# Kernel optimization log

Measured on AMD Instinct MI355X. Metric: run time of the kernel, lower is better.

## Reference

```python
import jax, jax.numpy as jnp
import numpy as np

B, C, D = 32768, 1000, 512
ALPHA, BETA = 1.0, 1.0
TEMPERATURE = 0.1


def setup_inputs() -> dict:
    key = jax.random.key(0)
    k1, k2, k3, k4 = jax.random.split(key, 4)
    return {
        "features_front": jax.random.normal(k1, (B, D), dtype=jnp.float32),
        "logits": jax.random.normal(k2, (B, C), dtype=jnp.float32),
        "labels": jax.random.randint(k3, (B,), 0, C, dtype=jnp.int64),
        "text_prototype": jax.random.normal(k4, (C, D), dtype=jnp.float32),
    }


def reference(features_front, logits, labels, text_prototype):
    num_class = text_prototype.shape[0]

    # F.cross_entropy (mean reduction)
    logp = jax.nn.log_softmax(logits, axis=-1)
    loss_ce = -jnp.mean(jnp.take_along_axis(logp, labels[:, None], axis=1)[:, 0])

    # F.normalize(prototypes, dim=1)
    norm = jnp.linalg.norm(text_prototype, axis=1, keepdims=True)
    prototypes = text_prototype / jnp.maximum(norm, 1e-12)

    # supervised contrastive term against class prototypes
    feat_dot_prototype = (features_front @ prototypes.T) / TEMPERATURE  # [B, C]
    logits_max = jax.lax.stop_gradient(jnp.max(feat_dot_prototype, axis=1, keepdims=True))
    lg = feat_dot_prototype - logits_max
    log_prob = lg - jnp.log(jnp.sum(jnp.exp(lg), axis=1, keepdims=True))
    mask = (labels[:, None] == jnp.arange(num_class)[None, :]).astype(log_prob.dtype)
    mean_log_prob_pos = jnp.sum(mask * log_prob, axis=1)
    simloss = -jnp.mean(mean_log_prob_pos)

    # prototype repulsion: sum_{i != j} exp(p_i . p_j) == masked exp-sum of Gram matrix
    gram = prototypes @ prototypes.T  # [C, C]
    offdiag = 1.0 - jnp.eye(num_class, dtype=gram.dtype)
    textloss = jnp.log(jnp.sum(jnp.exp(gram) * offdiag)) / num_class

    return ALPHA * simloss + BETA * loss_ce + textloss
```

## Files before the change

kernel.cpp:

```cpp
#include <hip/hip_runtime.h>
#include <math.h>

#define NB 32768
#define NC 1000
#define ND 512
#define NTILES 63
#define LOG2E 1.4426950408889634f
#define LN2 0.6931471805599453f
#define S2 14.426950408889634f
#define NBUCKET 64

typedef __attribute__((ext_vector_type(8))) short short8;
typedef __attribute__((ext_vector_type(4))) float f32x4;

__device__ __forceinline__ float fexp2(float x) {
    float r; asm("v_exp_f32 %0, %1" : "=v"(r) : "v"(x)); return r;
}
__device__ __forceinline__ float flog2(float x) {
    float r; asm("v_log_f32 %0, %1" : "=v"(r) : "v"(x)); return r;
}
__device__ __forceinline__ unsigned short bf16_rne(float f) {
    unsigned int u = __builtin_bit_cast(unsigned int, f);
    u += 0x7FFFu + ((u >> 16) & 1u);
    return (unsigned short)(u >> 16);
}
__device__ __forceinline__ short8 pack8f(float4 a, float4 b) {
    short8 s;
    s[0] = (short)bf16_rne(a.x); s[1] = (short)bf16_rne(a.y);
    s[2] = (short)bf16_rne(a.z); s[3] = (short)bf16_rne(a.w);
    s[4] = (short)bf16_rne(b.x); s[5] = (short)bf16_rne(b.y);
    s[6] = (short)bf16_rne(b.z); s[7] = (short)bf16_rne(b.w);
    return s;
}

__global__ __launch_bounds__(256) void norm_protos(const float* __restrict__ pro,
                                                   unsigned short* __restrict__ pbf) {
    const int row = blockIdx.x, t = threadIdx.x;
    const int tile = row >> 4, r = row & 15;
    const int kk = t >> 4, g = (t >> 2) & 3, slot = t & 3;
    unsigned int* dst = (unsigned int*)pbf +
        ((size_t)tile * 1024 + kk * 64 + g * 16 + r) * 4 + slot;
    if (row >= NC) { *dst = 0u; return; }
    const float* rp = pro + (size_t)row * ND;
    const float x0 = rp[2 * t], x1 = rp[2 * t + 1];
    float ss = x0 * x0 + x1 * x1;
#pragma unroll
    for (int o = 1; o < 64; o <<= 1) ss += __shfl_xor(ss, o, 64);
    __shared__ float part[4];
    if ((t & 63) == 0) part[t >> 6] = ss;
    __syncthreads();
    const float nrm = sqrtf(part[0] + part[1] + part[2] + part[3]);
    const float sc = 1.0f / fmaxf(nrm, 1e-12f);
    *dst = (unsigned int)bf16_rne(x0 * sc) | ((unsigned int)bf16_rne(x1 * sc) << 16);
}

#define TILE_BODY(P, CT)                                                            \
    do {                                                                            \
        f32x4 a0 = {0.f, 0.f, 0.f, 0.f}, a1 = {0.f, 0.f, 0.f, 0.f};                \
        _Pragma("unroll")                                                           \
        for (int kk = 0; kk < 16; ++kk) {                                           \
            a0 = __builtin_amdgcn_mfma_f32_16x16x32_bf16(P[kk], bf0[kk], a0, 0, 0, 0); \
            a1 = __builtin_amdgcn_mfma_f32_16x16x32_bf16(P[kk], bf1[kk], a1, 0, 0, 0); \
        }                                                                           \
        const int cbase = (CT) * 16 + g * 4;                                        \
        {                                                                           \
            float x[4];                                                            \
            _Pragma("unroll")                                                       \
            for (int rI = 0; rI < 4; ++rI) {                                        \
                const float v = a0[rI] * S2;                                        \
                x[rI] = (cbase + rI < NC) ? v : -INFINITY;                          \
                lv0 += (cbase + rI == lab0) ? v : 0.f;                              \
            }                                                                       \
            const float tmax = fmaxf(fmaxf(x[0], x[1]), fmaxf(x[2], x[3]));         \
            const float mn = fmaxf(m0, tmax);                                       \
            ls0 *= fexp2(m0 - mn);                                                  \
            m0 = mn;                                                                \
            ls0 += fexp2(x[0] - mn) + fexp2(x[1] - mn) + fexp2(x[2] - mn) + fexp2(x[3] - mn); \
        }                                                                           \
        {                                                                           \
            float x[4];                                                            \
            _Pragma("unroll")                                                       \
            for (int rI = 0; rI < 4; ++rI) {                                        \
                const float v = a1[rI] * S2;                                        \
                x[rI] = (cbase + rI < NC) ? v : -INFINITY;                          \
                lv1 += (cbase + rI == lab1) ? v : 0.f;                              \
            }                                                                       \
            const float tmax = fmaxf(fmaxf(x[0], x[1]), fmaxf(x[2], x[3]));         \
            const float mn = fmaxf(m1, tmax);                                       \
            ls1 *= fexp2(m1 - mn);                                                  \
            m1 = mn;                                                                \
            ls1 += fexp2(x[0] - mn) + fexp2(x[1] - mn) + fexp2(x[2] - mn) + fexp2(x[3] - mn); \
        }                                                                           \
    } while (0)

__global__ __launch_bounds__(256, 1) void main_kernel(const float* __restrict__ feat,
                                                      const float* __restrict__ logits,
                                                      const int* __restrict__ labels,
                                                      const unsigned short* __restrict__ pbf,
                                                      float* __restrict__ buckets) {
    __shared__ float wsum[4], wsumce[4];
    const int t = threadIdx.x;
    const int wid = t >> 6, lane = t & 63;
    const int r16 = lane & 15, g = lane >> 4;
    const int rowbase = blockIdx.x * 128 + wid * 32;
    const short8* frag = (const short8*)pbf;

    short8 PA[16], PB[16];
#pragma unroll
    for (int k = 0; k < 16; ++k) PA[k] = frag[k * 64 + lane];

    short8 bf0[16], bf1[16];
    {
        const float* f0 = feat + (size_t)(rowbase + r16) * ND + 8 * g;
        const float* f1 = f0 + 16 * ND;
#pragma unroll
        for (int kk = 0; kk < 16; ++kk) {
            bf0[kk] = pack8f(*(const float4*)(f0 + 32 * kk), *(const float4*)(f0 + 32 * kk + 4));
            bf1[kk] = pack8f(*(const float4*)(f1 + 32 * kk), *(const float4*)(f1 + 32 * kk + 4));
        }
    }
    int lab0 = labels[rowbase + r16];
    int lab1 = labels[rowbase + 16 + r16];
    lab0 = lab0 < 0 ? 0 : (lab0 > NC - 1 ? NC - 1 : lab0);
    lab1 = lab1 < 0 ? 0 : (lab1 > NC - 1 ? NC - 1 : lab1);

    float m0 = -INFINITY, ls0 = 0.f, lv0 = 0.f;
    float m1 = -INFINITY, ls1 = 0.f, lv1 = 0.f;

#pragma unroll 1
    for (int ct = 0; ct < 62; ct += 2) {
#pragma unroll
        for (int k = 0; k < 16; ++k) PB[k] = frag[(ct + 1) * 1024 + k * 64 + lane];
        TILE_BODY(PA, ct);
#pragma unroll
        for (int k = 0; k < 16; ++k) PA[k] = frag[(ct + 2) * 1024 + k * 64 + lane];
        TILE_BODY(PB, ct + 1);
    }
    TILE_BODY(PA, 62);

#pragma unroll
    for (int o = 16; o <= 32; o <<= 1) {
        {
            const float mo = __shfl_xor(m0, o, 64), lo = __shfl_xor(ls0, o, 64);
            lv0 += __shfl_xor(lv0, o, 64);
            const float mm = fmaxf(m0, mo);
            ls0 = ls0 * fexp2(m0 - mm) + lo * fexp2(mo - mm);
            m0 = mm;
        }
        {
            const float mo = __shfl_xor(m1, o, 64), lo = __shfl_xor(ls1, o, 64);
            lv1 += __shfl_xor(lv1, o, 64);
            const float mm = fmaxf(m1, mo);
            ls1 = ls1 * fexp2(m1 - mm) + lo * fexp2(mo - mm);
            m1 = mm;
        }
    }
    const float row0 = (m0 + flog2(ls0) - lv0) * LN2;
    const float row1 = (m1 + flog2(ls1) - lv1) * LN2;
    float mine = (row0 + row1) * (1.0f / (4.0f * (float)NB));
#pragma unroll
    for (int o = 1; o < 64; o <<= 1) mine += __shfl_xor(mine, o, 64);

    float localce = 0.f;
#pragma unroll 1
    for (int i = 0; i < 32; ++i) {
        const int row = rowbase + i;
        const float* rp = logits + (size_t)row * NC;
        float x[16];
#pragma unroll
        for (int j = 0; j < 4; ++j) {
            const int c0 = lane * 4 + j * 256;
            if (c0 < NC) {
                const float4 v = *(const float4*)(rp + c0);
                x[4 * j] = v.x * LOG2E; x[4 * j + 1] = v.y * LOG2E;
                x[4 * j + 2] = v.z * LOG2E; x[4 * j + 3] = v.w * LOG2E;
            } else {
                x[4 * j] = x[4 * j + 1] = x[4 * j + 2] = x[4 * j + 3] = -INFINITY;
            }
        }
        float m = -INFINITY;
#pragma unroll
        for (int i2 = 0; i2 < 16; ++i2) m = fmaxf(m, x[i2]);
#pragma unroll
        for (int o = 1; o < 64; o <<= 1) m = fmaxf(m, __shfl_xor(m, o, 64));
        float s = 0.f;
#pragma unroll
        for (int i2 = 0; i2 < 16; ++i2) s += fexp2(x[i2] - m);
#pragma unroll
        for (int o = 1; o < 64; o <<= 1) s += __shfl_xor(s, o, 64);
        int lab = labels[row];
        lab = lab < 0 ? 0 : (lab > NC - 1 ? NC - 1 : lab);
        localce += (m + flog2(s)) * LN2 - rp[lab];
    }

    if (lane == 0) { wsum[wid] = mine; wsumce[wid] = localce; }
    __syncthreads();
    if (t == 0) {
        const int b = (blockIdx.x & (NBUCKET - 1)) * 16;
        atomicAdd(buckets + b, wsum[0] + wsum[1] + wsum[2] + wsum[3]);
        atomicAdd(buckets + 1024 + b,
                  (wsumce[0] + wsumce[1] + wsumce[2] + wsumce[3]) * (1.0f / (float)NB));
    }
}

__global__ __launch_bounds__(256) void gram_kernel(const unsigned short* __restrict__ pbf,
                                                   float* __restrict__ buckets) {
    __shared__ float wsum[4];
    const int t = threadIdx.x;
    const int wid = t >> 6, lane = t & 63;
    const int r16 = lane & 15, g = lane >> 4;
    const int ct = blockIdx.y;
    const int btile = blockIdx.x * 4 + wid;
    const int irow = btile * 16 + r16;
    const short8* frag = (const short8*)pbf;

    short8 af[16], bf[16];
#pragma unroll
    for (int kk = 0; kk < 16; ++kk) {
        af[kk] = frag[(size_t)ct * 1024 + kk * 64 + lane];
        bf[kk] = frag[(size_t)btile * 1024 + kk * 64 + lane];
    }
    f32x4 dacc = {0.f, 0.f, 0.f, 0.f};
#pragma unroll
    for (int kk = 0; kk < 16; ++kk)
        dacc = __builtin_amdgcn_mfma_f32_16x16x32_bf16(af[kk], bf[kk], dacc, 0, 0, 0);

    float s = 0.f;
    if (irow < NC) {
        const int cbase = ct * 16 + g * 4;
#pragma unroll
        for (int rI = 0; rI < 4; ++rI) {
            const int j = cbase + rI;
            if (j < NC && j != irow) s += fexp2(dacc[rI] * LOG2E);
        }
    }
#pragma unroll
    for (int o = 1; o < 64; o <<= 1) s += __shfl_xor(s, o, 64);
    if (lane == 0) wsum[wid] = s;
    __syncthreads();
    if (t == 0)
        atomicAdd(buckets + ((blockIdx.x + 16 * blockIdx.y) & (NBUCKET - 1)) * 16,
                  wsum[0] + wsum[1] + wsum[2] + wsum[3]);
}

__global__ void combine_kernel(const float* __restrict__ a, float* __restrict__ out) {
    const int t = threadIdx.x;
    float s = a[t * 16], c = a[1024 + t * 16], gr = a[2048 + t * 16];
#pragma unroll
    for (int o = 1; o < 64; o <<= 1) {
        s += __shfl_xor(s, o, 64);
        c += __shfl_xor(c, o, 64);
        gr += __shfl_xor(gr, o, 64);
    }
    if (t == 0) out[0] = s + c + logf(gr) * (1.0f / (float)NC);
}

extern "C" void kernel_launch(void* const* d_in, const int* in_sizes, int n_in,
                              void* d_out, int out_size, void* d_ws, size_t ws_size,
                              hipStream_t stream) {
    const float* feat   = (const float*)d_in[0];
    const float* logits = (const float*)d_in[1];
    const int*   labels = (const int*)d_in[2];
    const float* pro    = (const float*)d_in[3];
    float* out = (float*)d_out;

    float* acc = (float*)d_ws;
    unsigned short* pbf = (unsigned short*)((char*)d_ws + 16384);

    hipMemsetAsync(d_ws, 0, 3072 * sizeof(float), stream);
    hipLaunchKernelGGL(norm_protos,    dim3(1024),     dim3(256), 0, stream, pro, pbf);
    hipLaunchKernelGGL(main_kernel,    dim3(NB / 128), dim3(256), 0, stream, feat, logits, labels, pbf, acc);
    hipLaunchKernelGGL(gram_kernel,    dim3(16, 63),   dim3(256), 0, stream, pbf, acc + 2048);
    hipLaunchKernelGGL(combine_kernel, dim3(1),        dim3(64),  0, stream, acc, out);
}
```

Before: 101.2 us.

## Halve rows per wave and split K-half prefetch to raise main kernel occupancy

Each wave now handles 16 feature rows instead of 32, and the grid doubles to NB/64 blocks. The prototype tile is prefetched in two K-halves of 8 fragments, with two partial MFMA accumulators summed afterwards. This cuts register use so launch bounds can ask for 2 blocks per CU, meant to hide memory latency better. The cross-entropy loop handles two rows per iteration for more ILP. The trade-off is that each prototype tile is reloaded by twice as many waves, and each MFMA chain is shorter.

```diff
diff --git a/kernel.cpp b/kernel.cpp
--- a/kernel.cpp
+++ b/kernel.cpp
@@ -54,46 +54,7 @@
     *dst = (unsigned int)bf16_rne(x0 * sc) | ((unsigned int)bf16_rne(x1 * sc) << 16);
 }
 
-#define TILE_BODY(P, CT)                                                            \
-    do {                                                                            \
-        f32x4 a0 = {0.f, 0.f, 0.f, 0.f}, a1 = {0.f, 0.f, 0.f, 0.f};                \
-        _Pragma("unroll")                                                           \
-        for (int kk = 0; kk < 16; ++kk) {                                           \
-            a0 = __builtin_amdgcn_mfma_f32_16x16x32_bf16(P[kk], bf0[kk], a0, 0, 0, 0); \
-            a1 = __builtin_amdgcn_mfma_f32_16x16x32_bf16(P[kk], bf1[kk], a1, 0, 0, 0); \
-        }                                                                           \
-        const int cbase = (CT) * 16 + g * 4;                                        \
-        {                                                                           \
-            float x[4];                                                            \
-            _Pragma("unroll")                                                       \
-            for (int rI = 0; rI < 4; ++rI) {                                        \
-                const float v = a0[rI] * S2;                                        \
-                x[rI] = (cbase + rI < NC) ? v : -INFINITY;                          \
-                lv0 += (cbase + rI == lab0) ? v : 0.f;                              \
-            }                                                                       \
-            const float tmax = fmaxf(fmaxf(x[0], x[1]), fmaxf(x[2], x[3]));         \
-            const float mn = fmaxf(m0, tmax);                                       \
-            ls0 *= fexp2(m0 - mn);                                                  \
-            m0 = mn;                                                                \
-            ls0 += fexp2(x[0] - mn) + fexp2(x[1] - mn) + fexp2(x[2] - mn) + fexp2(x[3] - mn); \
-        }                                                                           \
-        {                                                                           \
-            float x[4];                                                            \
-            _Pragma("unroll")                                                       \
-            for (int rI = 0; rI < 4; ++rI) {                                        \
-                const float v = a1[rI] * S2;                                        \
-                x[rI] = (cbase + rI < NC) ? v : -INFINITY;                          \
-                lv1 += (cbase + rI == lab1) ? v : 0.f;                              \
-            }                                                                       \
-            const float tmax = fmaxf(fmaxf(x[0], x[1]), fmaxf(x[2], x[3]));         \
-            const float mn = fmaxf(m1, tmax);                                       \
-            ls1 *= fexp2(m1 - mn);                                                  \
-            m1 = mn;                                                                \
-            ls1 += fexp2(x[0] - mn) + fexp2(x[1] - mn) + fexp2(x[2] - mn) + fexp2(x[3] - mn); \
-        }                                                                           \
-    } while (0)
-
-__global__ __launch_bounds__(256, 1) void main_kernel(const float* __restrict__ feat,
+__global__ __launch_bounds__(256, 2) void main_kernel(const float* __restrict__ feat,
                                                       const float* __restrict__ logits,
                                                       const int* __restrict__ labels,
                                                       const unsigned short* __restrict__ pbf,
@@ -102,95 +63,112 @@
     const int t = threadIdx.x;
     const int wid = t >> 6, lane = t & 63;
     const int r16 = lane & 15, g = lane >> 4;
-    const int rowbase = blockIdx.x * 128 + wid * 32;
+    const int rowbase = blockIdx.x * 64 + wid * 16;
     const short8* frag = (const short8*)pbf;
 
-    short8 PA[16], PB[16];
-#pragma unroll
-    for (int k = 0; k < 16; ++k) PA[k] = frag[k * 64 + lane];
-
-    short8 bf0[16], bf1[16];
+    short8 PA[8], PB[8];
+#pragma unroll
+    for (int k = 0; k < 8; ++k) PA[k] = frag[k * 64 + lane];
+
+    short8 bf[16];
     {
         const float* f0 = feat + (size_t)(rowbase + r16) * ND + 8 * g;
-        const float* f1 = f0 + 16 * ND;
-#pragma unroll
-        for (int kk = 0; kk < 16; ++kk) {
-            bf0[kk] = pack8f(*(const float4*)(f0 + 32 * kk), *(const float4*)(f0 + 32 * kk + 4));
-            bf1[kk] = pack8f(*(const float4*)(f1 + 32 * kk), *(const float4*)(f1 + 32 * kk + 4));
-        }
+#pragma unroll
+        for (int kk = 0; kk < 16; ++kk)
+            bf[kk] = pack8f(*(const float4*)(f0 + 32 * kk), *(const float4*)(f0 + 32 * kk + 4));
     }
     int lab0 = labels[rowbase + r16];
-    int lab1 = labels[rowbase + 16 + r16];
     lab0 = lab0 < 0 ? 0 : (lab0 > NC - 1 ? NC - 1 : lab0);
-    lab1 = lab1 < 0 ? 0 : (lab1 > NC - 1 ? NC - 1 : lab1);
 
     float m0 = -INFINITY, ls0 = 0.f, lv0 = 0.f;
-    float m1 = -INFINITY, ls1 = 0.f, lv1 = 0.f;
 
 #pragma unroll 1
-    for (int ct = 0; ct < 62; ct += 2) {
-#pragma unroll
-        for (int k = 0; k < 16; ++k) PB[k] = frag[(ct + 1) * 1024 + k * 64 + lane];
-        TILE_BODY(PA, ct);
-#pragma unroll
-        for (int k = 0; k < 16; ++k) PA[k] = frag[(ct + 2) * 1024 + k * 64 + lane];
-        TILE_BODY(PB, ct + 1);
-    }
-    TILE_BODY(PA, 62);
+    for (int ct = 0; ct < NTILES; ++ct) {
+        const int base = ct * 1024;
+#pragma unroll
+        for (int k = 0; k < 8; ++k) PB[k] = frag[base + (8 + k) * 64 + lane];
+        f32x4 aE = {0.f, 0.f, 0.f, 0.f};
+#pragma unroll
+        for (int k = 0; k < 8; ++k)
+            aE = __builtin_amdgcn_mfma_f32_16x16x32_bf16(PA[k], bf[k], aE, 0, 0, 0);
+        const int nbase = (ct < NTILES - 1) ? base + 1024 : base;
+#pragma unroll
+        for (int k = 0; k < 8; ++k) PA[k] = frag[nbase + k * 64 + lane];
+        f32x4 aO = {0.f, 0.f, 0.f, 0.f};
+#pragma unroll
+        for (int k = 0; k < 8; ++k)
+            aO = __builtin_amdgcn_mfma_f32_16x16x32_bf16(PB[k], bf[8 + k], aO, 0, 0, 0);
+
+        const int cbase = ct * 16 + g * 4;
+        float x[4];
+#pragma unroll
+        for (int rI = 0; rI < 4; ++rI) {
+            const float v = (aE[rI] + aO[rI]) * S2;
+            x[rI] = (cbase + rI < NC) ? v : -INFINITY;
+            lv0 += (cbase + rI == lab0) ? v : 0.f;
+        }
+        const float tmax = fmaxf(fmaxf(x[0], x[1]), fmaxf(x[2], x[3]));
+        const float mn = fmaxf(m0, tmax);
+        ls0 *= fexp2(m0 - mn);
+        m0 = mn;
+        ls0 += fexp2(x[0] - mn) + fexp2(x[1] - mn) + fexp2(x[2] - mn) + fexp2(x[3] - mn);
+    }
 
 #pragma unroll
     for (int o = 16; o <= 32; o <<= 1) {
-        {
-            const float mo = __shfl_xor(m0, o, 64), lo = __shfl_xor(ls0, o, 64);
-            lv0 += __shfl_xor(lv0, o, 64);
-            const float mm = fmaxf(m0, mo);
-            ls0 = ls0 * fexp2(m0 - mm) + lo * fexp2(mo - mm);
-            m0 = mm;
-        }
-        {
-            const float mo = __shfl_xor(m1, o, 64), lo = __shfl_xor(ls1, o, 64);
-            lv1 += __shfl_xor(lv1, o, 64);
-            const float mm = fmaxf(m1, mo);
-            ls1 = ls1 * fexp2(m1 - mm) + lo * fexp2(mo - mm);
-            m1 = mm;
-        }
+        const float mo = __shfl_xor(m0, o, 64), lo = __shfl_xor(ls0, o, 64);
+        lv0 += __shfl_xor(lv0, o, 64);
+        const float mm = fmaxf(m0, mo);
+        ls0 = ls0 * fexp2(m0 - mm) + lo * fexp2(mo - mm);
+        m0 = mm;
     }
     const float row0 = (m0 + flog2(ls0) - lv0) * LN2;
-    const float row1 = (m1 + flog2(ls1) - lv1) * LN2;
-    float mine = (row0 + row1) * (1.0f / (4.0f * (float)NB));
+    float mine = row0 * (1.0f / (4.0f * (float)NB));
 #pragma unroll
     for (int o = 1; o < 64; o <<= 1) mine += __shfl_xor(mine, o, 64);
 
     float localce = 0.f;
 #pragma unroll 1
-    for (int i = 0; i < 32; ++i) {
-        const int row = rowbase + i;
-        const float* rp = logits + (size_t)row * NC;
-        float x[16];
+    for (int i = 0; i < 16; i += 2) {
+        const float* rpA = logits + (size_t)(rowbase + i) * NC;
+        const float* rpB = rpA + NC;
+        float xa[16], xb[16];
 #pragma unroll
         for (int j = 0; j < 4; ++j) {
             const int c0 = lane * 4 + j * 256;
             if (c0 < NC) {
-                const float4 v = *(const float4*)(rp + c0);
-                x[4 * j] = v.x * LOG2E; x[4 * j + 1] = v.y * LOG2E;
-                x[4 * j + 2] = v.z * LOG2E; x[4 * j + 3] = v.w * LOG2E;
+                const float4 va = *(const float4*)(rpA + c0);
+                const float4 vb = *(const float4*)(rpB + c0);
+                xa[4 * j] = va.x * LOG2E; xa[4 * j + 1] = va.y * LOG2E;
+                xa[4 * j + 2] = va.z * LOG2E; xa[4 * j + 3] = va.w * LOG2E;
+                xb[4 * j] = vb.x * LOG2E; xb[4 * j + 1] = vb.y * LOG2E;
+                xb[4 * j + 2] = vb.z * LOG2E; xb[4 * j + 3] = vb.w * LOG2E;
             } else {
-                x[4 * j] = x[4 * j + 1] = x[4 * j + 2] = x[4 * j + 3] = -INFINITY;
+                xa[4 * j] = xa[4 * j + 1] = xa[4 * j + 2] = xa[4 * j + 3] = -INFINITY;
+                xb[4 * j] = xb[4 * j + 1] = xb[4 * j + 2] = xb[4 * j + 3] = -INFINITY;
             }
         }
-        float m = -INFINITY;
-#pragma unroll
-        for (int i2 = 0; i2 < 16; ++i2) m = fmaxf(m, x[i2]);
-#pragma unroll
-        for (int o = 1; o < 64; o <<= 1) m = fmaxf(m, __shfl_xor(m, o, 64));
-        float s = 0.f;
-#pragma unroll
-        for (int i2 = 0; i2 < 16; ++i2) s += fexp2(x[i2] - m);
-#pragma unroll
-        for (int o = 1; o < 64; o <<= 1) s += __shfl_xor(s, o, 64);
-        int lab = labels[row];
-        lab = lab < 0 ? 0 : (lab > NC - 1 ? NC - 1 : lab);
-        localce += (m + flog2(s)) * LN2 - rp[lab];
+        float mA = -INFINITY, mB = -INFINITY;
+#pragma unroll
+        for (int i2 = 0; i2 < 16; ++i2) { mA = fmaxf(mA, xa[i2]); mB = fmaxf(mB, xb[i2]); }
+#pragma unroll
+        for (int o = 1; o < 64; o <<= 1) {
+            mA = fmaxf(mA, __shfl_xor(mA, o, 64));
+            mB = fmaxf(mB, __shfl_xor(mB, o, 64));
+        }
+        float sA = 0.f, sB = 0.f;
+#pragma unroll
+        for (int i2 = 0; i2 < 16; ++i2) { sA += fexp2(xa[i2] - mA); sB += fexp2(xb[i2] - mB); }
+#pragma unroll
+        for (int o = 1; o < 64; o <<= 1) {
+            sA += __shfl_xor(sA, o, 64);
+            sB += __shfl_xor(sB, o, 64);
+        }
+        int labA = labels[rowbase + i], labB = labels[rowbase + i + 1];
+        labA = labA < 0 ? 0 : (labA > NC - 1 ? NC - 1 : labA);
+        labB = labB < 0 ? 0 : (labB > NC - 1 ? NC - 1 : labB);
+        localce += (mA + flog2(sA)) * LN2 - rpA[labA];
+        localce += (mB + flog2(sB)) * LN2 - rpB[labB];
     }
 
     if (lane == 0) { wsum[wid] = mine; wsumce[wid] = localce; }
@@ -214,16 +192,16 @@
     const int irow = btile * 16 + r16;
     const short8* frag = (const short8*)pbf;
 
-    short8 af[16], bf[16];
+    short8 af[16], bfr[16];
 #pragma unroll
     for (int kk = 0; kk < 16; ++kk) {
         af[kk] = frag[(size_t)ct * 1024 + kk * 64 + lane];
-        bf[kk] = frag[(size_t)btile * 1024 + kk * 64 + lane];
+        bfr[kk] = frag[(size_t)btile * 1024 + kk * 64 + lane];
     }
     f32x4 dacc = {0.f, 0.f, 0.f, 0.f};
 #pragma unroll
     for (int kk = 0; kk < 16; ++kk)
-        dacc = __builtin_amdgcn_mfma_f32_16x16x32_bf16(af[kk], bf[kk], dacc, 0, 0, 0);
+        dacc = __builtin_amdgcn_mfma_f32_16x16x32_bf16(af[kk], bfr[kk], dacc, 0, 0, 0);
 
     float s = 0.f;
     if (irow < NC) {
@@ -268,8 +246,8 @@
     unsigned short* pbf = (unsigned short*)((char*)d_ws + 16384);
 
     hipMemsetAsync(d_ws, 0, 3072 * sizeof(float), stream);
-    hipLaunchKernelGGL(norm_protos,    dim3(1024),     dim3(256), 0, stream, pro, pbf);
-    hipLaunchKernelGGL(main_kernel,    dim3(NB / 128), dim3(256), 0, stream, feat, logits, labels, pbf, acc);
-    hipLaunchKernelGGL(gram_kernel,    dim3(16, 63),   dim3(256), 0, stream, pbf, acc + 2048);
-    hipLaunchKernelGGL(combine_kernel, dim3(1),        dim3(64),  0, stream, acc, out);
-}
+    hipLaunchKernelGGL(norm_protos,    dim3(1024),    dim3(256), 0, stream, pro, pbf);
+    hipLaunchKernelGGL(main_kernel,    dim3(NB / 64), dim3(256), 0, stream, feat, logits, labels, pbf, acc);
+    hipLaunchKernelGGL(gram_kernel,    dim3(16, 63),  dim3(256), 0, stream, pbf, acc + 2048);
+    hipLaunchKernelGGL(combine_kernel, dim3(1),       dim3(64),  0, stream, acc, out);
+}
```

Result: slower. 205.8 us (+103.5%).

## Process four CE rows per wave with 16-lane groups and add per-tile barrier

Applied to the files above, without the earlier changes.

The cross-entropy tail now assigns each 16-lane quarter of a wave its own logits row. This cuts the full 64-lane shuffle reductions per row down to 4-step reductions and handles four rows per iteration, increasing memory-level parallelism. It also adds a __syncthreads inside the main prototype tile loop, presumably to keep the waves in step so their shared prototype fragment reads stay cache-friendly. The barrier can add stall time, and a variable is renamed in the gram kernel.

```diff
diff --git a/kernel.cpp b/kernel.cpp
--- a/kernel.cpp
+++ b/kernel.cpp
@@ -135,6 +135,7 @@
 #pragma unroll
         for (int k = 0; k < 16; ++k) PA[k] = frag[(ct + 2) * 1024 + k * 64 + lane];
         TILE_BODY(PB, ct + 1);
+        __syncthreads();
     }
     TILE_BODY(PA, 62);
 
@@ -161,37 +162,49 @@
 #pragma unroll
     for (int o = 1; o < 64; o <<= 1) mine += __shfl_xor(mine, o, 64);
 
+    const int q4 = lane >> 4, l16 = lane & 15;
     float localce = 0.f;
 #pragma unroll 1
-    for (int i = 0; i < 32; ++i) {
-        const int row = rowbase + i;
+    for (int i = 0; i < 8; ++i) {
+        const int row = rowbase + 4 * i + q4;
         const float* rp = logits + (size_t)row * NC;
-        float x[16];
-#pragma unroll
-        for (int j = 0; j < 4; ++j) {
-            const int c0 = lane * 4 + j * 256;
-            if (c0 < NC) {
-                const float4 v = *(const float4*)(rp + c0);
-                x[4 * j] = v.x * LOG2E; x[4 * j + 1] = v.y * LOG2E;
-                x[4 * j + 2] = v.z * LOG2E; x[4 * j + 3] = v.w * LOG2E;
-            } else {
-                x[4 * j] = x[4 * j + 1] = x[4 * j + 2] = x[4 * j + 3] = -INFINITY;
-            }
+        const float4* rp4 = (const float4*)rp;
+        float4 xs[16];
+#pragma unroll
+        for (int j = 0; j < 15; ++j) {
+            const float4 v = rp4[l16 + 16 * j];
+            xs[j].x = v.x * LOG2E; xs[j].y = v.y * LOG2E;
+            xs[j].z = v.z * LOG2E; xs[j].w = v.w * LOG2E;
+        }
+        if (l16 < 10) {
+            const float4 v = rp4[l16 + 240];
+            xs[15].x = v.x * LOG2E; xs[15].y = v.y * LOG2E;
+            xs[15].z = v.z * LOG2E; xs[15].w = v.w * LOG2E;
+        } else {
+            xs[15].x = xs[15].y = xs[15].z = xs[15].w = -INFINITY;
         }
         float m = -INFINITY;
 #pragma unroll
-        for (int i2 = 0; i2 < 16; ++i2) m = fmaxf(m, x[i2]);
-#pragma unroll
-        for (int o = 1; o < 64; o <<= 1) m = fmaxf(m, __shfl_xor(m, o, 64));
+        for (int j = 0; j < 16; ++j)
+            m = fmaxf(m, fmaxf(fmaxf(xs[j].x, xs[j].y), fmaxf(xs[j].z, xs[j].w)));
+#pragma unroll
+        for (int o = 1; o <= 8; o <<= 1) m = fmaxf(m, __shfl_xor(m, o, 64));
         float s = 0.f;
 #pragma unroll
-        for (int i2 = 0; i2 < 16; ++i2) s += fexp2(x[i2] - m);
-#pragma unroll
-        for (int o = 1; o < 64; o <<= 1) s += __shfl_xor(s, o, 64);
-        int lab = labels[row];
-        lab = lab < 0 ? 0 : (lab > NC - 1 ? NC - 1 : lab);
-        localce += (m + flog2(s)) * LN2 - rp[lab];
-    }
+        for (int j = 0; j < 16; ++j)
+            s += fexp2(xs[j].x - m) + fexp2(xs[j].y - m) +
+                 fexp2(xs[j].z - m) + fexp2(xs[j].w - m);
+#pragma unroll
+        for (int o = 1; o <= 8; o <<= 1) s += __shfl_xor(s, o, 64);
+        if (l16 == 0) {
+            int lab = labels[row];
+            lab = lab < 0 ? 0 : (lab > NC - 1 ? NC - 1 : lab);
+            localce += (m + flog2(s)) * LN2 - rp[lab];
+        }
+    }
+
+#pragma unroll
+    for (int o = 1; o < 64; o <<= 1) localce += __shfl_xor(localce, o, 64);
 
     if (lane == 0) { wsum[wid] = mine; wsumce[wid] = localce; }
     __syncthreads();
@@ -214,16 +227,16 @@
     const int irow = btile * 16 + r16;
     const short8* frag = (const short8*)pbf;
 
-    short8 af[16], bf[16];
+    short8 af[16], bfr[16];
 #pragma unroll
     for (int kk = 0; kk < 16; ++kk) {
         af[kk] = frag[(size_t)ct * 1024 + kk * 64 + lane];
-        bf[kk] = frag[(size_t)btile * 1024 + kk * 64 + lane];
+        bfr[kk] = frag[(size_t)btile * 1024 + kk * 64 + lane];
     }
     f32x4 dacc = {0.f, 0.f, 0.f, 0.f};
 #pragma unroll
     for (int kk = 0; kk < 16; ++kk)
-        dacc = __builtin_amdgcn_mfma_f32_16x16x32_bf16(af[kk], bf[kk], dacc, 0, 0, 0);
+        dacc = __builtin_amdgcn_mfma_f32_16x16x32_bf16(af[kk], bfr[kk], dacc, 0, 0, 0);
 
     float s = 0.f;
     if (irow < NC) {
```

Measured after the change: 94.89 us. 6.2% less time.
